# Performance work log

Hardware: AMD Instinct MI355X
Metric: run time of the kernel (lower is better)

Reference implementation:

```python
import jax, jax.numpy as jnp
import numpy as np

B, S, H, FFN, E = 2, 2048, 1024, 4096, 8

def setup_inputs() -> dict:
    key = jax.random.key(0)
    k0, k1, k2, k3 = jax.random.split(key, 4)
    return {
        "hidden_states": jax.random.normal(k0, (B, S, H), dtype=jnp.float32),
        "Wr": jax.random.normal(k1, (H, E), dtype=jnp.float32) * 0.02,
        "br": jnp.zeros((E,), dtype=jnp.float32),
        "W1": jax.random.normal(k2, (E, H, FFN), dtype=jnp.float32) * 0.02,
        "W2": jax.random.normal(k3, (E, FFN, H), dtype=jnp.float32) * 0.02,
    }

def reference(hidden_states, Wr, br, W1, W2):
    b, s, h = hidden_states.shape
    x = hidden_states.reshape(-1, h)                      # [T, H]
    # sinkhorn routing branch in forward: sigmoid activation then top-1
    route = jax.nn.sigmoid(x @ Wr + br)                   # [T, E]
    max_prob = jnp.max(route, axis=1, keepdims=True)      # [T, 1]
    max_ind = jnp.argmax(route, axis=1)                   # [T] int
    out = jnp.zeros_like(x)
    n_experts = Wr.shape[1]
    for e in range(n_experts):  # small fixed expert set
        mask = (max_ind == e)[:, None].astype(x.dtype)    # [T, 1] dispatch mask
        # expert MLP: fc2(gelu(fc1(x))), no bias (add_bias_linear=False)
        y = jax.nn.gelu(x @ W1[e], approximate=False) @ W2[e]  # [T, H]
        out = out + mask * y                              # scatter-combine
    out = out * max_prob                                  # scale by router prob
    return out.reshape(b, s, h)
```

## Files before the change

kernel.cpp:

```cpp
#include <hip/hip_runtime.h>
#include <hip/hip_bf16.h>
#include <math.h>

#define TOK 4096
#define HD 1024
#define FD 4096
#define NE 8

typedef __attribute__((ext_vector_type(4))) float f32x4;
typedef __attribute__((ext_vector_type(8))) short s16x8;
typedef __attribute__((ext_vector_type(4))) unsigned int u32x4;

typedef const __attribute__((address_space(1))) void g_void;
typedef __attribute__((address_space(3))) void lds_void;

__device__ __forceinline__ unsigned short f2bf(float f) {
    union { float f; unsigned u; } v; v.f = f;
    unsigned r = v.u + 0x7FFFu + ((v.u >> 16) & 1u);
    return (unsigned short)(r >> 16);
}

__device__ __forceinline__ unsigned cvt2(float a, float b) {
    unsigned r;
    asm("v_cvt_pk_bf16_f32 %0, %1, %2" : "=v"(r) : "v"(a), "v"(b));
    return r;
}

__global__ void router_kernel(const float* __restrict__ x, const float* __restrict__ Wr,
                              const float* __restrict__ br, int* __restrict__ counts,
                              int* __restrict__ tlist, float* __restrict__ mprob,
                              unsigned short* __restrict__ xb) {
    const int lane = threadIdx.x & 63;
    const int t = blockIdx.x * 4 + (threadIdx.x >> 6);
    const float* xr = x + (size_t)t * HD;
    unsigned short* xbr = xb + (size_t)t * HD;
    float acc[NE];
#pragma unroll
    for (int e = 0; e < NE; ++e) acc[e] = 0.f;
    for (int h = lane; h < HD; h += 64) {
        float xv = xr[h];
        xbr[h] = f2bf(xv);
        f32x4 w0 = *(const f32x4*)(Wr + h * NE);
        f32x4 w1 = *(const f32x4*)(Wr + h * NE + 4);
        acc[0] += xv * w0.x; acc[1] += xv * w0.y; acc[2] += xv * w0.z; acc[3] += xv * w0.w;
        acc[4] += xv * w1.x; acc[5] += xv * w1.y; acc[6] += xv * w1.z; acc[7] += xv * w1.w;
    }
#pragma unroll
    for (int off = 32; off >= 1; off >>= 1)
#pragma unroll
        for (int e = 0; e < NE; ++e) acc[e] += __shfl_down(acc[e], off, 64);
    if (lane == 0) {
        float best = -1.f; int bi = 0;
#pragma unroll
        for (int e = 0; e < NE; ++e) {
            float r = 1.f / (1.f + expf(-(acc[e] + br[e])));
            if (r > best) { best = r; bi = e; }
        }
        mprob[t] = best;
        int pos = atomicAdd(&counts[bi], 1);
        tlist[bi * TOK + pos] = t;
    }
}

template<int K, bool FC1, int KSPLIT>
__global__ __launch_bounds__(256, 2)
void expert_gemm(const unsigned short* __restrict__ Asrc, const float* __restrict__ Wsrc,
                 const int* __restrict__ counts, const int* __restrict__ tlist,
                 const float* __restrict__ mprob,
                 unsigned short* __restrict__ inter, float* __restrict__ out) {
    constexpr int NDIM = FC1 ? FD : HD;
    constexpr int KC = K / KSPLIT;
    constexpr int NT = KC / 64;
    const int e  = (KSPLIT == 1) ? blockIdx.z : ((int)blockIdx.z & (NE - 1));
    const int ks = (KSPLIT == 1) ? 0 : ((int)blockIdx.z >> 3);
    const int kbase = ks * KC;
    const int cnt = counts[e];
    const int m0 = blockIdx.y * 128;
    if (m0 >= cnt) return;
    const int n0 = blockIdx.x * 128;

    __shared__ unsigned short Al[2][128 * 64];
    __shared__ float Braw[64 * 128];
    __shared__ unsigned short Bl[128 * 64];

    const int tid = threadIdx.x;
    const int lane = tid & 63;
    const int wave = tid >> 6;

    const unsigned short* aptr[4];
    {
        int lr = lane >> 3, g = lane & 7;
#pragma unroll
        for (int it = 0; it < 4; ++it) {
            int r = wave * 32 + it * 8 + lr;
            int kg = (g - r) & 7;
            int m = m0 + r;
            int tk = (m < cnt) ? tlist[e * TOK + m] : 0;
            aptr[it] = Asrc + (size_t)tk * K + kbase + kg * 8;
        }
    }
    const float* bptr = Wsrc + ((size_t)e * K + kbase + wave * 16 + (lane >> 5)) * NDIM
                        + n0 + ((lane & 31) << 2);

    const int wrow = (wave >> 1) << 6;
    const int wcol = (wave & 1) << 6;
    const int lm = lane & 15, quad = lane >> 4;
    const int cg = tid >> 3;
    const int gg = tid & 7;

    f32x4 acc[4][4] = {};

#pragma unroll
    for (int it = 0; it < 4; ++it)
        __builtin_amdgcn_global_load_lds((g_void*)aptr[it],
            (lds_void*)&Al[0][wave * 2048 + it * 512], 16, 0, 0);
#pragma unroll
    for (int L = 0; L < 8; ++L)
        __builtin_amdgcn_global_load_lds((g_void*)(bptr + (size_t)(L * 2) * NDIM),
            (lds_void*)&Braw[(wave * 16 + L * 2) * 128], 16, 0, 0);

    for (int t = 0; t < NT; ++t) {
        const int buf = t & 1;
        asm volatile("s_waitcnt vmcnt(0) lgkmcnt(0)\n\ts_barrier" ::: "memory");

        {
            f32x4 v[8];
#pragma unroll
            for (int j = 0; j < 8; ++j)
                v[j] = *(const f32x4*)&Braw[(gg * 8 + j) * 128 + (cg << 2)];
#pragma unroll
            for (int i = 0; i < 4; ++i) {
                int n = (cg << 2) + i;
                u32x4 q;
                q.x = cvt2(v[0][i], v[1][i]);
                q.y = cvt2(v[2][i], v[3][i]);
                q.z = cvt2(v[4][i], v[5][i]);
                q.w = cvt2(v[6][i], v[7][i]);
                *(u32x4*)&Bl[(n << 6) + (((gg + n) & 7) << 3)] = q;
            }
        }
        asm volatile("s_waitcnt lgkmcnt(0)\n\ts_barrier" ::: "memory");

        if (t + 1 < NT) {
#pragma unroll
            for (int it = 0; it < 4; ++it) {
                aptr[it] += 64;
                __builtin_amdgcn_global_load_lds((g_void*)aptr[it],
                    (lds_void*)&Al[buf ^ 1][wave * 2048 + it * 512], 16, 0, 0);
            }
            bptr += (size_t)64 * NDIM;
#pragma unroll
            for (int L = 0; L < 8; ++L)
                __builtin_amdgcn_global_load_lds((g_void*)(bptr + (size_t)(L * 2) * NDIM),
                    (lds_void*)&Braw[(wave * 16 + L * 2) * 128], 16, 0, 0);
            __builtin_amdgcn_sched_barrier(0);
        }

#pragma unroll
        for (int kt = 0; kt < 2; ++kt) {
            s16x8 af[4], bf[4];
            int gk = (kt << 2) + quad;
#pragma unroll
            for (int mt = 0; mt < 4; ++mt) {
                int m = wrow + (mt << 4) + lm;
                af[mt] = *(const s16x8*)&Al[buf][(m << 6) + (((gk + m) & 7) << 3)];
            }
#pragma unroll
            for (int nt = 0; nt < 4; ++nt) {
                int n = wcol + (nt << 4) + lm;
                bf[nt] = *(const s16x8*)&Bl[(n << 6) + (((gk + n) & 7) << 3)];
            }
#pragma unroll
            for (int mt = 0; mt < 4; ++mt)
#pragma unroll
                for (int nt = 0; nt < 4; ++nt)
                    acc[mt][nt] = __builtin_amdgcn_mfma_f32_16x16x32_bf16(
                        af[mt], bf[nt], acc[mt][nt], 0, 0, 0);
        }
    }

#pragma unroll
    for (int mt = 0; mt < 4; ++mt) {
#pragma unroll
        for (int r = 0; r < 4; ++r) {
            int row = wrow + (mt << 4) + (quad << 2) + r;
            if (m0 + row >= cnt) continue;
            int tk = tlist[e * TOK + m0 + row];
            int colb = n0 + wcol + lm;
            if constexpr (FC1) {
#pragma unroll
                for (int nt = 0; nt < 4; ++nt) {
                    float v = acc[mt][nt][r];
                    float g = 0.5f * v * (1.f + erff(v * 0.70710678f));
                    inter[(size_t)tk * FD + colb + (nt << 4)] = f2bf(g);
                }
            } else {
                float p = mprob[tk];
#pragma unroll
                for (int nt = 0; nt < 4; ++nt)
                    atomicAdd(&out[(size_t)tk * HD + colb + (nt << 4)], acc[mt][nt][r] * p);
            }
        }
    }
}

extern "C" void kernel_launch(void* const* d_in, const int* in_sizes, int n_in,
                              void* d_out, int out_size, void* d_ws, size_t ws_size,
                              hipStream_t stream) {
    const float* x  = (const float*)d_in[0];
    const float* Wr = (const float*)d_in[1];
    const float* br = (const float*)d_in[2];
    const float* W1 = (const float*)d_in[3];
    const float* W2 = (const float*)d_in[4];
    float* out = (float*)d_out;

    char* ws = (char*)d_ws;
    int* counts           = (int*)ws;
    float* mprob          = (float*)(ws + 256);
    int* tlist            = (int*)(ws + 16640);
    unsigned short* xb    = (unsigned short*)(ws + 147712);
    unsigned short* inter = (unsigned short*)(ws + 8536320);

    hipMemsetAsync(counts, 0, NE * sizeof(int), stream);
    hipMemsetAsync(out, 0, (size_t)out_size * sizeof(float), stream);
    router_kernel<<<TOK / 4, 256, 0, stream>>>(x, Wr, br, counts, tlist, mprob, xb);

    expert_gemm<HD, true, 1><<<dim3(FD / 128, TOK / 128, NE), 256, 0, stream>>>(
        xb, W1, counts, tlist, mprob, inter, nullptr);

    expert_gemm<FD, false, 2><<<dim3(HD / 128, TOK / 128, NE * 2), 256, 0, stream>>>(
        inter, W2, counts, tlist, mprob, nullptr, out);
}
```

Measured before the change: 549.2 us.

## Load B via registers into triple-buffered LDS, read A fragments directly from global

The per-tile pipeline is restructured. Weight tiles are now loaded into registers, converted to bf16 and written into a triple-buffered LDS ring, with the next tile's global load issued early. A operand fragments are read straight from global memory into MFMA registers instead of being staged in LDS, which removes one barrier per iteration and shrinks LDS use. Occupancy is raised to 3 blocks per CU and FC2 moves to 4-way K split. The risks are uncoalesced, latency-exposed direct global A loads, higher register pressure, and more atomic traffic into the output.

```diff
diff --git a/kernel.cpp b/kernel.cpp
--- a/kernel.cpp
+++ b/kernel.cpp
@@ -10,9 +10,6 @@
 typedef __attribute__((ext_vector_type(4))) float f32x4;
 typedef __attribute__((ext_vector_type(8))) short s16x8;
 typedef __attribute__((ext_vector_type(4))) unsigned int u32x4;
-
-typedef const __attribute__((address_space(1))) void g_void;
-typedef __attribute__((address_space(3))) void lds_void;
 
 __device__ __forceinline__ unsigned short f2bf(float f) {
     union { float f; unsigned u; } v; v.f = f;
@@ -63,7 +60,7 @@
 }
 
 template<int K, bool FC1, int KSPLIT>
-__global__ __launch_bounds__(256, 2)
+__global__ __launch_bounds__(256, 3)
 void expert_gemm(const unsigned short* __restrict__ Asrc, const float* __restrict__ Wsrc,
                  const int* __restrict__ counts, const int* __restrict__ tlist,
                  const float* __restrict__ mprob,
@@ -71,7 +68,7 @@
     constexpr int NDIM = FC1 ? FD : HD;
     constexpr int KC = K / KSPLIT;
     constexpr int NT = KC / 64;
-    const int e  = (KSPLIT == 1) ? blockIdx.z : ((int)blockIdx.z & (NE - 1));
+    const int e  = (KSPLIT == 1) ? (int)blockIdx.z : ((int)blockIdx.z & (NE - 1));
     const int ks = (KSPLIT == 1) ? 0 : ((int)blockIdx.z >> 3);
     const int kbase = ks * KC;
     const int cnt = counts[e];
@@ -79,96 +76,72 @@
     if (m0 >= cnt) return;
     const int n0 = blockIdx.x * 128;
 
-    __shared__ unsigned short Al[2][128 * 64];
-    __shared__ float Braw[64 * 128];
-    __shared__ unsigned short Bl[128 * 64];
+    __shared__ unsigned short Bl[3][128 * 64];
 
     const int tid = threadIdx.x;
     const int lane = tid & 63;
     const int wave = tid >> 6;
-
-    const unsigned short* aptr[4];
-    {
-        int lr = lane >> 3, g = lane & 7;
-#pragma unroll
-        for (int it = 0; it < 4; ++it) {
-            int r = wave * 32 + it * 8 + lr;
-            int kg = (g - r) & 7;
-            int m = m0 + r;
-            int tk = (m < cnt) ? tlist[e * TOK + m] : 0;
-            aptr[it] = Asrc + (size_t)tk * K + kbase + kg * 8;
-        }
-    }
-    const float* bptr = Wsrc + ((size_t)e * K + kbase + wave * 16 + (lane >> 5)) * NDIM
-                        + n0 + ((lane & 31) << 2);
-
     const int wrow = (wave >> 1) << 6;
     const int wcol = (wave & 1) << 6;
     const int lm = lane & 15, quad = lane >> 4;
+
+    const unsigned short* aPtr[4];
+#pragma unroll
+    for (int mt = 0; mt < 4; ++mt) {
+        int m = m0 + wrow + (mt << 4) + lm;
+        int tk = (m < cnt) ? tlist[e * TOK + m] : 0;
+        aPtr[mt] = Asrc + (size_t)tk * K + kbase + (quad << 3);
+    }
+
+    const int gg = tid & 7;
     const int cg = tid >> 3;
-    const int gg = tid & 7;
+    const float* bPtr = Wsrc + ((size_t)e * K + kbase + (gg << 3)) * NDIM + n0 + (cg << 2);
+
+    f32x4 breg[8];
+    auto loadB = [&]() {
+#pragma unroll
+        for (int j = 0; j < 8; ++j) breg[j] = *(const f32x4*)(bPtr + (size_t)j * NDIM);
+        bPtr += (size_t)64 * NDIM;
+    };
+    auto cvtB = [&](unsigned short* __restrict__ dst) {
+#pragma unroll
+        for (int i = 0; i < 4; ++i) {
+            int n = (cg << 2) + i;
+            u32x4 q;
+            q.x = cvt2(breg[0][i], breg[1][i]);
+            q.y = cvt2(breg[2][i], breg[3][i]);
+            q.z = cvt2(breg[4][i], breg[5][i]);
+            q.w = cvt2(breg[6][i], breg[7][i]);
+            *(u32x4*)&dst[(n << 6) + (((gg + n) & 7) << 3)] = q;
+        }
+    };
 
     f32x4 acc[4][4] = {};
 
-#pragma unroll
-    for (int it = 0; it < 4; ++it)
-        __builtin_amdgcn_global_load_lds((g_void*)aptr[it],
-            (lds_void*)&Al[0][wave * 2048 + it * 512], 16, 0, 0);
-#pragma unroll
-    for (int L = 0; L < 8; ++L)
-        __builtin_amdgcn_global_load_lds((g_void*)(bptr + (size_t)(L * 2) * NDIM),
-            (lds_void*)&Braw[(wave * 16 + L * 2) * 128], 16, 0, 0);
-
-    for (int t = 0; t < NT; ++t) {
-        const int buf = t & 1;
-        asm volatile("s_waitcnt vmcnt(0) lgkmcnt(0)\n\ts_barrier" ::: "memory");
-
-        {
-            f32x4 v[8];
-#pragma unroll
-            for (int j = 0; j < 8; ++j)
-                v[j] = *(const f32x4*)&Braw[(gg * 8 + j) * 128 + (cg << 2)];
-#pragma unroll
-            for (int i = 0; i < 4; ++i) {
-                int n = (cg << 2) + i;
-                u32x4 q;
-                q.x = cvt2(v[0][i], v[1][i]);
-                q.y = cvt2(v[2][i], v[3][i]);
-                q.z = cvt2(v[4][i], v[5][i]);
-                q.w = cvt2(v[6][i], v[7][i]);
-                *(u32x4*)&Bl[(n << 6) + (((gg + n) & 7) << 3)] = q;
-            }
+    loadB();
+    cvtB(&Bl[0][0]);
+    loadB();
+
+    int bufC = 0;
+    for (int tt = 0; tt < NT; ++tt) {
+        int bufW = bufC + 1; if (bufW == 3) bufW = 0;
+        if (tt + 1 < NT) {
+            cvtB(&Bl[bufW][0]);
+            if (tt + 2 < NT) loadB();
         }
         asm volatile("s_waitcnt lgkmcnt(0)\n\ts_barrier" ::: "memory");
-
-        if (t + 1 < NT) {
-#pragma unroll
-            for (int it = 0; it < 4; ++it) {
-                aptr[it] += 64;
-                __builtin_amdgcn_global_load_lds((g_void*)aptr[it],
-                    (lds_void*)&Al[buf ^ 1][wave * 2048 + it * 512], 16, 0, 0);
-            }
-            bptr += (size_t)64 * NDIM;
-#pragma unroll
-            for (int L = 0; L < 8; ++L)
-                __builtin_amdgcn_global_load_lds((g_void*)(bptr + (size_t)(L * 2) * NDIM),
-                    (lds_void*)&Braw[(wave * 16 + L * 2) * 128], 16, 0, 0);
-            __builtin_amdgcn_sched_barrier(0);
-        }
-
+        const unsigned short* blc = &Bl[bufC][0];
 #pragma unroll
         for (int kt = 0; kt < 2; ++kt) {
             s16x8 af[4], bf[4];
-            int gk = (kt << 2) + quad;
-#pragma unroll
-            for (int mt = 0; mt < 4; ++mt) {
-                int m = wrow + (mt << 4) + lm;
-                af[mt] = *(const s16x8*)&Al[buf][(m << 6) + (((gk + m) & 7) << 3)];
-            }
+#pragma unroll
+            for (int mt = 0; mt < 4; ++mt)
+                af[mt] = *(const s16x8*)(aPtr[mt] + (kt << 5));
 #pragma unroll
             for (int nt = 0; nt < 4; ++nt) {
                 int n = wcol + (nt << 4) + lm;
-                bf[nt] = *(const s16x8*)&Bl[(n << 6) + (((gk + n) & 7) << 3)];
+                int gk = (kt << 2) + quad;
+                bf[nt] = *(const s16x8*)&blc[(n << 6) + (((gk + n) & 7) << 3)];
             }
 #pragma unroll
             for (int mt = 0; mt < 4; ++mt)
@@ -177,6 +150,9 @@
                     acc[mt][nt] = __builtin_amdgcn_mfma_f32_16x16x32_bf16(
                         af[mt], bf[nt], acc[mt][nt], 0, 0, 0);
         }
+#pragma unroll
+        for (int mt = 0; mt < 4; ++mt) aPtr[mt] += 64;
+        bufC = bufW;
     }
 
 #pragma unroll
@@ -228,6 +204,6 @@
     expert_gemm<HD, true, 1><<<dim3(FD / 128, TOK / 128, NE), 256, 0, stream>>>(
         xb, W1, counts, tlist, mprob, inter, nullptr);
 
-    expert_gemm<FD, false, 2><<<dim3(HD / 128, TOK / 128, NE * 2), 256, 0, stream>>>(
+    expert_gemm<FD, false, 4><<<dim3(HD / 128, TOK / 128, NE * 4), 256, 0, stream>>>(
         inter, W2, counts, tlist, mprob, nullptr, out);
 }
```

Result: slower. 647.4 us (+17.9%).

## Pre-transpose and cast expert weights to bf16 before each GEMM

Applied to the files above, without the earlier changes.

Adds a transpose_cast kernel that converts each expert weight matrix to bf16 in N-major layout in workspace before its GEMM. The GEMM then loads both operands directly into double-buffered LDS, dropping the per-tile fp32-to-bf16 conversion and one barrier per iteration. The FC2 split-K factor also rises from 2 to 4. The cost is an extra full pass over the weights each call and more atomic adds on the output.

```diff
diff --git a/kernel.cpp b/kernel.cpp
--- a/kernel.cpp
+++ b/kernel.cpp
@@ -62,16 +62,56 @@
     }
 }
 
+template<int K, int N>
+__global__ __launch_bounds__(256)
+void transpose_cast(const float* __restrict__ src, unsigned short* __restrict__ dst) {
+    __shared__ unsigned short T[128 * 64];
+    const int e  = blockIdx.z;
+    const int n0 = blockIdx.x * 128;
+    const int k0 = blockIdx.y * 64;
+    const int tid = threadIdx.x;
+    {
+        const int gg = tid & 7;
+        const int cg = tid >> 3;
+        const float* sp = src + ((size_t)e * K + k0 + gg * 8) * N + n0 + (cg << 2);
+        f32x4 v[8];
+#pragma unroll
+        for (int j = 0; j < 8; ++j) v[j] = *(const f32x4*)(sp + (size_t)j * N);
+#pragma unroll
+        for (int i = 0; i < 4; ++i) {
+            int n = (cg << 2) + i;
+            u32x4 q;
+            q.x = cvt2(v[0][i], v[1][i]);
+            q.y = cvt2(v[2][i], v[3][i]);
+            q.z = cvt2(v[4][i], v[5][i]);
+            q.w = cvt2(v[6][i], v[7][i]);
+            *(u32x4*)&T[(n << 6) + (((gg + n) & 7) << 3)] = q;
+        }
+    }
+    __syncthreads();
+    {
+        const int n = tid >> 1;
+        const int half = tid & 1;
+        unsigned short* op = dst + ((size_t)e * N + n0 + n) * K + k0 + half * 32;
+#pragma unroll
+        for (int j = 0; j < 4; ++j) {
+            int kg = half * 4 + j;
+            s16x8 c = *(const s16x8*)&T[(n << 6) + (((kg + n) & 7) << 3)];
+            *(s16x8*)(op + j * 8) = c;
+        }
+    }
+}
+
 template<int K, bool FC1, int KSPLIT>
 __global__ __launch_bounds__(256, 2)
-void expert_gemm(const unsigned short* __restrict__ Asrc, const float* __restrict__ Wsrc,
+void expert_gemm(const unsigned short* __restrict__ Asrc, const unsigned short* __restrict__ Wt,
                  const int* __restrict__ counts, const int* __restrict__ tlist,
                  const float* __restrict__ mprob,
                  unsigned short* __restrict__ inter, float* __restrict__ out) {
     constexpr int NDIM = FC1 ? FD : HD;
     constexpr int KC = K / KSPLIT;
     constexpr int NT = KC / 64;
-    const int e  = (KSPLIT == 1) ? blockIdx.z : ((int)blockIdx.z & (NE - 1));
+    const int e  = (KSPLIT == 1) ? (int)blockIdx.z : ((int)blockIdx.z & (NE - 1));
     const int ks = (KSPLIT == 1) ? 0 : ((int)blockIdx.z >> 3);
     const int kbase = ks * KC;
     const int cnt = counts[e];
@@ -80,14 +120,14 @@
     const int n0 = blockIdx.x * 128;
 
     __shared__ unsigned short Al[2][128 * 64];
-    __shared__ float Braw[64 * 128];
-    __shared__ unsigned short Bl[128 * 64];
+    __shared__ unsigned short Bl[2][128 * 64];
 
     const int tid = threadIdx.x;
     const int lane = tid & 63;
     const int wave = tid >> 6;
 
     const unsigned short* aptr[4];
+    const unsigned short* bptr[4];
     {
         int lr = lane >> 3, g = lane & 7;
 #pragma unroll
@@ -97,65 +137,42 @@
             int m = m0 + r;
             int tk = (m < cnt) ? tlist[e * TOK + m] : 0;
             aptr[it] = Asrc + (size_t)tk * K + kbase + kg * 8;
-        }
-    }
-    const float* bptr = Wsrc + ((size_t)e * K + kbase + wave * 16 + (lane >> 5)) * NDIM
-                        + n0 + ((lane & 31) << 2);
+            bptr[it] = Wt + ((size_t)e * NDIM + n0 + r) * K + kbase + kg * 8;
+        }
+    }
 
     const int wrow = (wave >> 1) << 6;
     const int wcol = (wave & 1) << 6;
     const int lm = lane & 15, quad = lane >> 4;
-    const int cg = tid >> 3;
-    const int gg = tid & 7;
 
     f32x4 acc[4][4] = {};
 
 #pragma unroll
-    for (int it = 0; it < 4; ++it)
+    for (int it = 0; it < 4; ++it) {
         __builtin_amdgcn_global_load_lds((g_void*)aptr[it],
             (lds_void*)&Al[0][wave * 2048 + it * 512], 16, 0, 0);
-#pragma unroll
-    for (int L = 0; L < 8; ++L)
-        __builtin_amdgcn_global_load_lds((g_void*)(bptr + (size_t)(L * 2) * NDIM),
-            (lds_void*)&Braw[(wave * 16 + L * 2) * 128], 16, 0, 0);
+        __builtin_amdgcn_global_load_lds((g_void*)bptr[it],
+            (lds_void*)&Bl[0][wave * 2048 + it * 512], 16, 0, 0);
+        aptr[it] += 64; bptr[it] += 64;
+    }
 
     for (int t = 0; t < NT; ++t) {
         const int buf = t & 1;
-        asm volatile("s_waitcnt vmcnt(0) lgkmcnt(0)\n\ts_barrier" ::: "memory");
-
-        {
-            f32x4 v[8];
-#pragma unroll
-            for (int j = 0; j < 8; ++j)
-                v[j] = *(const f32x4*)&Braw[(gg * 8 + j) * 128 + (cg << 2)];
-#pragma unroll
-            for (int i = 0; i < 4; ++i) {
-                int n = (cg << 2) + i;
-                u32x4 q;
-                q.x = cvt2(v[0][i], v[1][i]);
-                q.y = cvt2(v[2][i], v[3][i]);
-                q.z = cvt2(v[4][i], v[5][i]);
-                q.w = cvt2(v[6][i], v[7][i]);
-                *(u32x4*)&Bl[(n << 6) + (((gg + n) & 7) << 3)] = q;
-            }
-        }
-        asm volatile("s_waitcnt lgkmcnt(0)\n\ts_barrier" ::: "memory");
-
+        asm volatile("s_waitcnt vmcnt(0)" ::: "memory");
+        __builtin_amdgcn_s_barrier();
         if (t + 1 < NT) {
 #pragma unroll
             for (int it = 0; it < 4; ++it) {
-                aptr[it] += 64;
                 __builtin_amdgcn_global_load_lds((g_void*)aptr[it],
                     (lds_void*)&Al[buf ^ 1][wave * 2048 + it * 512], 16, 0, 0);
-            }
-            bptr += (size_t)64 * NDIM;
-#pragma unroll
-            for (int L = 0; L < 8; ++L)
-                __builtin_amdgcn_global_load_lds((g_void*)(bptr + (size_t)(L * 2) * NDIM),
-                    (lds_void*)&Braw[(wave * 16 + L * 2) * 128], 16, 0, 0);
+                __builtin_amdgcn_global_load_lds((g_void*)bptr[it],
+                    (lds_void*)&Bl[buf ^ 1][wave * 2048 + it * 512], 16, 0, 0);
+                aptr[it] += 64; bptr[it] += 64;
+            }
             __builtin_amdgcn_sched_barrier(0);
         }
-
+        const unsigned short* Ab = &Al[buf][0];
+        const unsigned short* Bb = &Bl[buf][0];
 #pragma unroll
         for (int kt = 0; kt < 2; ++kt) {
             s16x8 af[4], bf[4];
@@ -163,12 +180,12 @@
 #pragma unroll
             for (int mt = 0; mt < 4; ++mt) {
                 int m = wrow + (mt << 4) + lm;
-                af[mt] = *(const s16x8*)&Al[buf][(m << 6) + (((gk + m) & 7) << 3)];
+                af[mt] = *(const s16x8*)&Ab[(m << 6) + (((gk + m) & 7) << 3)];
             }
 #pragma unroll
             for (int nt = 0; nt < 4; ++nt) {
                 int n = wcol + (nt << 4) + lm;
-                bf[nt] = *(const s16x8*)&Bl[(n << 6) + (((gk + n) & 7) << 3)];
+                bf[nt] = *(const s16x8*)&Bb[(n << 6) + (((gk + n) & 7) << 3)];
             }
 #pragma unroll
             for (int mt = 0; mt < 4; ++mt)
@@ -220,14 +237,17 @@
     int* tlist            = (int*)(ws + 16640);
     unsigned short* xb    = (unsigned short*)(ws + 147712);
     unsigned short* inter = (unsigned short*)(ws + 8536320);
+    unsigned short* Wt    = (unsigned short*)(ws + 42090752);
 
     hipMemsetAsync(counts, 0, NE * sizeof(int), stream);
     hipMemsetAsync(out, 0, (size_t)out_size * sizeof(float), stream);
     router_kernel<<<TOK / 4, 256, 0, stream>>>(x, Wr, br, counts, tlist, mprob, xb);
 
+    transpose_cast<HD, FD><<<dim3(FD / 128, HD / 64, NE), 256, 0, stream>>>(W1, Wt);
     expert_gemm<HD, true, 1><<<dim3(FD / 128, TOK / 128, NE), 256, 0, stream>>>(
-        xb, W1, counts, tlist, mprob, inter, nullptr);
-
-    expert_gemm<FD, false, 2><<<dim3(HD / 128, TOK / 128, NE * 2), 256, 0, stream>>>(
-        inter, W2, counts, tlist, mprob, nullptr, out);
-}
+        xb, Wt, counts, tlist, mprob, inter, nullptr);
+
+    transpose_cast<FD, HD><<<dim3(HD / 128, FD / 64, NE), 256, 0, stream>>>(W2, Wt);
+    expert_gemm<FD, false, 4><<<dim3(HD / 128, TOK / 128, NE * 4), 256, 0, stream>>>(
+        inter, Wt, counts, tlist, mprob, nullptr, out);
+}
```

After: 546.5 us. No clear change (-0.5%).
